# Kernel tuning notes

Hardware: AMD Instinct MI355X
Metric: run time of the kernel (lower is better)

## Reference

```python
import jax, jax.numpy as jnp
import numpy as np
from jax import lax

WS = (4, 8, 8)        # window_size (D,H,W)
DIM = 128
HEADS = 4
HD = DIM // HEADS      # 32
SCALE = HD ** -0.5     # swinv1, lif neuron -> head_dim**-0.5
TAU = 2.0
VTH = 1.0
ALPHA = 2.0            # ATan surrogate width


def _rel_pos_index(ws):
    # static numpy computation of relative_position_index, shape (N, N)
    coords = np.stack(np.meshgrid(np.arange(ws[0]), np.arange(ws[1]), np.arange(ws[2]), indexing='ij'))
    cf = coords.reshape(3, -1)                      # (3, N)
    rel = (cf[:, :, None] - cf[:, None, :]).transpose(1, 2, 0).astype(np.int64)  # (N,N,3)
    rel[:, :, 0] += ws[0] - 1
    rel[:, :, 1] += ws[1] - 1
    rel[:, :, 2] += ws[2] - 1
    rel[:, :, 0] *= (2 * ws[1] - 1) * (2 * ws[2] - 1)
    rel[:, :, 1] *= 2 * ws[2] - 1
    return rel.sum(-1)

RPI = _rel_pos_index(WS)  # (N, N) int


@jax.custom_vjp
def spike(x):
    return (x >= 0.0).astype(x.dtype)

def _spike_fwd(x):
    return spike(x), x

def _spike_bwd(x, g):
    # ATan surrogate gradient (spikingjelly default)
    return (g * (ALPHA / (2.0 * (1.0 + (np.pi / 2.0 * ALPHA * x) ** 2))),)

spike.defvjp(_spike_fwd, _spike_bwd)


def lif(x):
    # multi-step LIF over leading time axis: v' = v + (x - v)/tau, hard reset to 0
    def step(v, xt):
        v = v + (xt - v) / TAU
        s = spike(v - VTH)
        return v * (1.0 - s), s
    return lax.scan(step, jnp.zeros_like(x[0]), x)[1]


def setup_inputs() -> dict:
    key = jax.random.key(0)
    ks = jax.random.split(key, 7)
    x = jax.random.normal(ks[0], (WS[0], 256, WS[1], WS[2], DIM), dtype=jnp.float32)
    Wq = jax.random.normal(ks[1], (DIM, DIM), dtype=jnp.float32) * 0.02
    Wk = jax.random.normal(ks[2], (DIM, DIM), dtype=jnp.float32) * 0.02
    Wv = jax.random.normal(ks[3], (DIM, DIM), dtype=jnp.float32) * 0.02
    rpb_table = jax.random.normal(ks[4], ((2 * WS[0] - 1) * (2 * WS[1] - 1) * (2 * WS[2] - 1), HEADS), dtype=jnp.float32) * 0.02
    Wproj = jax.random.normal(ks[5], (DIM, DIM), dtype=jnp.float32) * 0.02
    bproj = jax.random.normal(ks[6], (DIM,), dtype=jnp.float32) * 0.02
    return {"x": x, "Wq": Wq, "Wk": Wk, "Wv": Wv, "rpb_table": rpb_table, "Wproj": Wproj, "bproj": bproj}


def reference(x, Wq, Wk, Wv, rpb_table, Wproj, bproj):
    T, B_, H, W, C = x.shape
    N = T * H * W
    # QKV: linear (no bias) -> spiking neuron over time axis
    q = lif(jnp.einsum('tbhwc,dc->tbhwd', x, Wq))
    k = lif(jnp.einsum('tbhwc,dc->tbhwd', x, Wk))
    v = lif(jnp.einsum('tbhwc,dc->tbhwd', x, Wv))
    # literal row-major reshape as in torch: (T,B_,H,W,C) -> (B_, heads, N, hd)
    q = q.reshape(B_, HEADS, N, HD)
    k = k.reshape(B_, HEADS, N, HD)
    v = v.reshape(B_, HEADS, N, HD)
    # scaled QK^T (NO softmax in the original forward)
    attn = jnp.einsum('bhnd,bhmd->bhnm', q * SCALE, k)
    rpb = rpb_table[RPI.reshape(-1)].reshape(N, N, HEADS).transpose(2, 0, 1)  # (heads,N,N)
    attn = attn + rpb[None]
    out = jnp.einsum('bhnm,bhmd->bhnd', attn, v)
    out = out.reshape(B_, HEADS, T, H, W, HD).transpose(2, 0, 3, 4, 1, 5).reshape(T, B_, H, W, C)
    out = jnp.einsum('tbhwc,dc->tbhwd', out, Wproj) + bproj
    out = lif(out).reshape(B_, N, C)
    return (out, attn)
```

## Files before the change

kernel.cpp:

```cpp
#include <hip/hip_runtime.h>
#include <hip/hip_bf16.h>


typedef __attribute__((ext_vector_type(8))) short bf16x8;
typedef __attribute__((ext_vector_type(4))) float f32x4;

#define MFMA16(a, b, c) __builtin_amdgcn_mfma_f32_16x16x32_bf16((a), (b), (c), 0, 0, 0)

#define BAR_LDS()                                                \
    do {                                                         \
        asm volatile("s_waitcnt lgkmcnt(0)" ::: "memory");       \
        __builtin_amdgcn_s_barrier();                            \
    } while (0)

__device__ __forceinline__ unsigned short f2bf(float f) {
    union { __hip_bfloat16 h; unsigned short u; } cv;
    cv.h = __float2bfloat16(f);
    return cv.u;
}

__device__ __forceinline__ void cvt8_store(unsigned short* dst, const float* src) {
    float4 f0 = *(const float4*)(src);
    float4 f1 = *(const float4*)(src + 4);
    unsigned short h[8];
    h[0] = f2bf(f0.x); h[1] = f2bf(f0.y); h[2] = f2bf(f0.z); h[3] = f2bf(f0.w);
    h[4] = f2bf(f1.x); h[5] = f2bf(f1.y); h[6] = f2bf(f1.z); h[7] = f2bf(f1.w);
    *(uint4*)dst = *(const uint4*)h;
}

__global__ __launch_bounds__(256) void k_qkv_lif(
    const float* __restrict__ x,
    const float* __restrict__ Wq,
    const float* __restrict__ Wk,
    const float* __restrict__ Wv,
    const float* __restrict__ tbl,
    unsigned int* __restrict__ qbits,
    unsigned int* __restrict__ kbits,
    unsigned int* __restrict__ vbits,
    float* __restrict__ rpbx)
{
    if (blockIdx.y == 3) {
        int base = blockIdx.x * 1024 + threadIdx.x * 4;
        int hh = base >> 16;
        int n = (base >> 8) & 255, m0 = base & 255;
        int zn = n >> 6, yn = (n >> 3) & 7, xn = n & 7;
        float4 o;
#pragma unroll
        for (int i = 0; i < 4; ++i) {
            int m = m0 + i;
            int zm = m >> 6, ym = (m >> 3) & 7, xm = m & 7;
            int ri = (zn - zm + 3) * 225 + (yn - ym + 7) * 15 + (xn - xm + 7);
            ((float*)&o)[i] = tbl[ri * 4 + hh];
        }
        *(float4*)&rpbx[base] = o;
        return;
    }

    __shared__ unsigned short Wl[128 * 136];
    __shared__ unsigned short Xl[64 * 136];

    const int tid = threadIdx.x;
    const int wv = tid >> 6, lane = tid & 63;
    const int l15 = lane & 15, lh = lane >> 4;
    const int wsel = blockIdx.y;
    const float* W = (wsel == 0) ? Wq : (wsel == 1) ? Wk : Wv;
    unsigned int* bits = (wsel == 0) ? qbits : (wsel == 1) ? kbits : vbits;
    const int B = blockIdx.x;

    {
#pragma unroll
        for (int i = 0; i < 8; ++i) {
            int e = i * 2048 + tid * 8;
            int r = e >> 7, cc = e & 127;
            cvt8_store(&Wl[r * 136 + cc], W + r * 128 + cc);
        }
    }

    f32x4 vst[8];
#pragma unroll
    for (int nt = 0; nt < 8; ++nt) vst[nt] = (f32x4){0.f, 0.f, 0.f, 0.f};

    for (int t = 0; t < 4; ++t) {
        BAR_LDS();
        const float* xg = x + t * 2097152 + B * 8192;
#pragma unroll
        for (int i = 0; i < 4; ++i) {
            int e = i * 2048 + tid * 8;
            int r = e >> 7, cc = e & 127;
            cvt8_store(&Xl[r * 136 + cc], xg + r * 128 + cc);
        }
        BAR_LDS();

        f32x4 acc[8];
#pragma unroll
        for (int nt = 0; nt < 8; ++nt) acc[nt] = (f32x4){0.f, 0.f, 0.f, 0.f};
#pragma unroll
        for (int kk = 0; kk < 4; ++kk) {
            bf16x8 a = *(const bf16x8*)&Xl[(wv * 16 + l15) * 136 + kk * 32 + lh * 8];
#pragma unroll
            for (int nt = 0; nt < 8; ++nt) {
                bf16x8 b = *(const bf16x8*)&Wl[(nt * 16 + l15) * 136 + kk * 32 + lh * 8];
                acc[nt] = MFMA16(a, b, acc[nt]);
            }
        }
        unsigned short sp[8][4];
#pragma unroll
        for (int nt = 0; nt < 8; ++nt) {
#pragma unroll
            for (int reg = 0; reg < 4; ++reg) {
                float y = acc[nt][reg];
                float v = vst[nt][reg];
                v = v + (y - v) * 0.5f;
                float s = (v >= 1.0f) ? 1.0f : 0.0f;
                vst[nt][reg] = v * (1.0f - s);
                sp[nt][reg] = (s != 0.0f) ? (unsigned short)1 : (unsigned short)0;
            }
        }
        BAR_LDS();
#pragma unroll
        for (int nt = 0; nt < 8; ++nt)
#pragma unroll
            for (int reg = 0; reg < 4; ++reg)
                Xl[(wv * 16 + lh * 4 + reg) * 136 + nt * 16 + l15] = sp[nt][reg];
        BAR_LDS();
        {
            const unsigned short* rowp = &Xl[(tid >> 2) * 136 + (tid & 3) * 32];
            unsigned int mask = 0;
#pragma unroll
            for (int j8 = 0; j8 < 4; ++j8) {
                uint4 u = *(const uint4*)(rowp + j8 * 8);
                int base = j8 * 8;
                if (u.x & 0xFFFFu) mask |= 1u << (base + 0);
                if (u.x >> 16)     mask |= 1u << (base + 1);
                if (u.y & 0xFFFFu) mask |= 1u << (base + 2);
                if (u.y >> 16)     mask |= 1u << (base + 3);
                if (u.z & 0xFFFFu) mask |= 1u << (base + 4);
                if (u.z >> 16)     mask |= 1u << (base + 5);
                if (u.w & 0xFFFFu) mask |= 1u << (base + 6);
                if (u.w >> 16)     mask |= 1u << (base + 7);
            }
            bits[(t * 256 + B) * 256 + tid] = mask;
        }
    }
}

__global__ __launch_bounds__(256) void k_attn(
    const unsigned int* __restrict__ qbits,
    const unsigned int* __restrict__ kbits,
    const unsigned int* __restrict__ vbits,
    const float* __restrict__ rpbx,
    float* __restrict__ attn_out,
    unsigned short* __restrict__ o_ws)
{
    __shared__ unsigned int  qb[256];
    __shared__ unsigned short vT[32 * 264];
    __shared__ unsigned short attnL[32 * 264];

    const int tid = threadIdx.x;
    const int wv = tid >> 6, lane = tid & 63;
    const int l15 = lane & 15, lh = lane >> 4;
    const int g = blockIdx.x, hh = g & 3;

    qb[tid] = qbits[g * 256 + tid];
    uint4 km = *(const uint4*)&kbits[g * 256 + (tid & 63) * 4];
    {
        unsigned int vb = vbits[g * 256 + tid];
#pragma unroll
        for (int d = 0; d < 32; ++d)
            vT[d * 264 + tid] = ((vb >> d) & 1u) ? (unsigned short)0x3F80
                                                 : (unsigned short)0;
    }
    BAR_LDS();

    const float SC = 0.17677669529663687f;
    float* attn_b = attn_out + (size_t)g * 65536;
    const float* rp = rpbx + hh * 65536;
    unsigned short* ob = o_ws + g * 8192;
    const int rg = wv, m0 = (tid & 63) * 4;
    const int rt = wv >> 1, nh = wv & 1;

    for (int c = 0; c < 8; ++c) {
#pragma unroll
        for (int j = 0; j < 8; ++j) {
            int n = c * 32 + j * 4 + rg;
            unsigned int qn = qb[n];
            float4 rp4 = *(const float4*)&rp[n * 256 + m0];
            f32x4 av;
            av.x = (float)__popc(qn & km.x) * SC + rp4.x;
            av.y = (float)__popc(qn & km.y) * SC + rp4.y;
            av.z = (float)__popc(qn & km.z) * SC + rp4.z;
            av.w = (float)__popc(qn & km.w) * SC + rp4.w;
            __builtin_nontemporal_store(av, (f32x4*)(attn_b + n * 256 + m0));
            unsigned int p0 = (unsigned int)f2bf(av.x) | ((unsigned int)f2bf(av.y) << 16);
            unsigned int p1 = (unsigned int)f2bf(av.z) | ((unsigned int)f2bf(av.w) << 16);
            uint2 pk; pk.x = p0; pk.y = p1;
            *(uint2*)&attnL[(j * 4 + rg) * 264 + m0] = pk;
        }
        BAR_LDS();
        f32x4 oc = (f32x4){0.f, 0.f, 0.f, 0.f};
#pragma unroll
        for (int kk = 0; kk < 8; ++kk) {
            bf16x8 a = *(const bf16x8*)&attnL[(rt * 16 + l15) * 264 + kk * 32 + lh * 8];
            bf16x8 b = *(const bf16x8*)&vT[(nh * 16 + l15) * 264 + kk * 32 + lh * 8];
            oc = MFMA16(a, b, oc);
        }
#pragma unroll
        for (int reg = 0; reg < 4; ++reg) {
            int n = c * 32 + rt * 16 + lh * 4 + reg;
            ob[n * 32 + nh * 16 + l15] = f2bf(oc[reg]);
        }
        BAR_LDS();
    }
}

__global__ __launch_bounds__(256) void k_proj_lif(
    const unsigned short* __restrict__ o_ws,
    const float* __restrict__ Wp,
    const float* __restrict__ bp,
    float* __restrict__ out0)
{
    __shared__ unsigned short Wl[128 * 136];
    __shared__ unsigned short Al[64 * 136];

    const int tid = threadIdx.x;
    const int wv = tid >> 6, lane = tid & 63;
    const int l15 = lane & 15, lh = lane >> 4;
    const int b = blockIdx.x;

    {
#pragma unroll
        for (int i = 0; i < 8; ++i) {
            int e = i * 2048 + tid * 8;
            int r = e >> 7, cc = e & 127;
            cvt8_store(&Wl[r * 136 + cc], Wp + r * 128 + cc);
        }
    }

    float biasf[2];
#pragma unroll
    for (int ntl = 0; ntl < 2; ++ntl)
        biasf[ntl] = bp[(wv * 2 + ntl) * 16 + l15];

    const unsigned short* ob = o_ws + b * 32768;

    for (int c = 0; c < 4; ++c) {
        BAR_LDS();
#pragma unroll
        for (int i = 0; i < 4; ++i) {
            int e = i * 2048 + tid * 8;
            int lr2 = e >> 7, cc = e & 127;
            int t2 = lr2 >> 4, rit = lr2 & 15;
            int hhh = cc >> 5, hd = cc & 31;
            int n = t2 * 64 + c * 16 + rit;
            *(uint4*)&Al[lr2 * 136 + cc] =
                *(const uint4*)(ob + (hhh * 256 + n) * 32 + hd);
        }
        BAR_LDS();

        f32x4 acc[4][2];
#pragma unroll
        for (int t2 = 0; t2 < 4; ++t2)
#pragma unroll
            for (int ntl = 0; ntl < 2; ++ntl)
                acc[t2][ntl] = (f32x4){0.f, 0.f, 0.f, 0.f};
#pragma unroll
        for (int kk = 0; kk < 4; ++kk) {
            bf16x8 a[4];
#pragma unroll
            for (int t2 = 0; t2 < 4; ++t2)
                a[t2] = *(const bf16x8*)&Al[(t2 * 16 + l15) * 136 + kk * 32 + lh * 8];
#pragma unroll
            for (int ntl = 0; ntl < 2; ++ntl) {
                bf16x8 bb = *(const bf16x8*)&Wl[((wv * 2 + ntl) * 16 + l15) * 136 + kk * 32 + lh * 8];
#pragma unroll
                for (int t2 = 0; t2 < 4; ++t2)
                    acc[t2][ntl] = MFMA16(a[t2], bb, acc[t2][ntl]);
            }
        }
#pragma unroll
        for (int ntl = 0; ntl < 2; ++ntl) {
            int d = (wv * 2 + ntl) * 16 + l15;
#pragma unroll
            for (int reg = 0; reg < 4; ++reg) {
                int hw = c * 16 + lh * 4 + reg;
                float v = 0.f;
#pragma unroll
                for (int t2 = 0; t2 < 4; ++t2) {
                    float y = acc[t2][ntl][reg] + biasf[ntl];
                    v = v + (y - v) * 0.5f;
                    float s = (v >= 1.0f) ? 1.0f : 0.0f;
                    v = v * (1.0f - s);
                    __builtin_nontemporal_store(
                        s, out0 + t2 * 2097152 + b * 8192 + hw * 128 + d);
                }
            }
        }
    }
}

extern "C" void kernel_launch(void* const* d_in, const int* in_sizes, int n_in,
                              void* d_out, int out_size, void* d_ws, size_t ws_size,
                              hipStream_t stream)
{
    const float* x   = (const float*)d_in[0];
    const float* Wq  = (const float*)d_in[1];
    const float* Wk  = (const float*)d_in[2];
    const float* Wv  = (const float*)d_in[3];
    const float* tbl = (const float*)d_in[4];
    const float* Wp  = (const float*)d_in[5];
    const float* bp  = (const float*)d_in[6];

    float* out0 = (float*)d_out;
    float* attn = out0 + 8388608;

    unsigned short* o_ws = (unsigned short*)d_ws;
    unsigned int* qbits = (unsigned int*)(o_ws + 8388608);
    unsigned int* kbits = qbits + 262144;
    unsigned int* vbits = kbits + 262144;
    float* rpbx = (float*)(vbits + 262144);

    k_qkv_lif<<<dim3(256, 4), 256, 0, stream>>>(x, Wq, Wk, Wv, tbl,
                                                qbits, kbits, vbits, rpbx);
    k_attn<<<1024, 256, 0, stream>>>(qbits, kbits, vbits, rpbx, attn, o_ws);
    k_proj_lif<<<256, 256, 0, stream>>>(o_ws, Wp, bp, out0);
}
```

Before: 351.6 us.

## Compute relative position bias in-kernel from LDS table instead of expanded buffer

Drops the pre-expanded 4x256x256 relative-position-bias buffer written by the QKV kernel. Each attention block now loads its head's 1575-entry slice of the table into LDS and computes the bias index arithmetically per element. The q bitmasks are read directly from global memory with a wave-uniform row index, so they no longer go through LDS. This removes 1 MB of writes plus repeated global reads of the bias, at the cost of scattered LDS reads and more integer index work per element.

After: 355.3 us. Within noise of the previous version (+1.0%).

```diff
diff --git a/kernel.cpp b/kernel.cpp
--- a/kernel.cpp
+++ b/kernel.cpp
@@ -33,29 +33,10 @@
     const float* __restrict__ Wq,
     const float* __restrict__ Wk,
     const float* __restrict__ Wv,
-    const float* __restrict__ tbl,
     unsigned int* __restrict__ qbits,
     unsigned int* __restrict__ kbits,
-    unsigned int* __restrict__ vbits,
-    float* __restrict__ rpbx)
+    unsigned int* __restrict__ vbits)
 {
-    if (blockIdx.y == 3) {
-        int base = blockIdx.x * 1024 + threadIdx.x * 4;
-        int hh = base >> 16;
-        int n = (base >> 8) & 255, m0 = base & 255;
-        int zn = n >> 6, yn = (n >> 3) & 7, xn = n & 7;
-        float4 o;
-#pragma unroll
-        for (int i = 0; i < 4; ++i) {
-            int m = m0 + i;
-            int zm = m >> 6, ym = (m >> 3) & 7, xm = m & 7;
-            int ri = (zn - zm + 3) * 225 + (yn - ym + 7) * 15 + (xn - xm + 7);
-            ((float*)&o)[i] = tbl[ri * 4 + hh];
-        }
-        *(float4*)&rpbx[base] = o;
-        return;
-    }
-
     __shared__ unsigned short Wl[128 * 136];
     __shared__ unsigned short Xl[64 * 136];
 
@@ -148,20 +129,22 @@
     const unsigned int* __restrict__ qbits,
     const unsigned int* __restrict__ kbits,
     const unsigned int* __restrict__ vbits,
-    const float* __restrict__ rpbx,
+    const float* __restrict__ tbl,
     float* __restrict__ attn_out,
     unsigned short* __restrict__ o_ws)
 {
-    __shared__ unsigned int  qb[256];
     __shared__ unsigned short vT[32 * 264];
     __shared__ unsigned short attnL[32 * 264];
+    __shared__ float tblL[1575];
 
     const int tid = threadIdx.x;
     const int wv = tid >> 6, lane = tid & 63;
     const int l15 = lane & 15, lh = lane >> 4;
     const int g = blockIdx.x, hh = g & 3;
 
-    qb[tid] = qbits[g * 256 + tid];
+    for (int i = tid; i < 1575; i += 256)
+        tblL[i] = tbl[i * 4 + hh];
+
     uint4 km = *(const uint4*)&kbits[g * 256 + (tid & 63) * 4];
     {
         unsigned int vb = vbits[g * 256 + tid];
@@ -170,31 +153,40 @@
             vT[d * 264 + tid] = ((vb >> d) & 1u) ? (unsigned short)0x3F80
                                                  : (unsigned short)0;
     }
+
+    const int m0 = (tid & 63) * 4;
+    int dm[4];
+#pragma unroll
+    for (int i = 0; i < 4; ++i) {
+        int m = m0 + i;
+        dm[i] = (m >> 6) * 225 + ((m >> 3) & 7) * 15 + (m & 7);
+    }
+
     BAR_LDS();
 
     const float SC = 0.17677669529663687f;
     float* attn_b = attn_out + (size_t)g * 65536;
-    const float* rp = rpbx + hh * 65536;
     unsigned short* ob = o_ws + g * 8192;
-    const int rg = wv, m0 = (tid & 63) * 4;
+    const int rowb = __builtin_amdgcn_readfirstlane(wv * 8);
     const int rt = wv >> 1, nh = wv & 1;
 
     for (int c = 0; c < 8; ++c) {
 #pragma unroll
         for (int j = 0; j < 8; ++j) {
-            int n = c * 32 + j * 4 + rg;
-            unsigned int qn = qb[n];
-            float4 rp4 = *(const float4*)&rp[n * 256 + m0];
+            int n = c * 32 + rowb + j;
+            unsigned int qn = qbits[g * 256 + n];
+            int zn = n >> 6, yn = (n >> 3) & 7, xn = n & 7;
+            int basei = zn * 225 + yn * 15 + xn + 787;
             f32x4 av;
-            av.x = (float)__popc(qn & km.x) * SC + rp4.x;
-            av.y = (float)__popc(qn & km.y) * SC + rp4.y;
-            av.z = (float)__popc(qn & km.z) * SC + rp4.z;
-            av.w = (float)__popc(qn & km.w) * SC + rp4.w;
+            av.x = (float)__popc(qn & km.x) * SC + tblL[basei - dm[0]];
+            av.y = (float)__popc(qn & km.y) * SC + tblL[basei - dm[1]];
+            av.z = (float)__popc(qn & km.z) * SC + tblL[basei - dm[2]];
+            av.w = (float)__popc(qn & km.w) * SC + tblL[basei - dm[3]];
             __builtin_nontemporal_store(av, (f32x4*)(attn_b + n * 256 + m0));
             unsigned int p0 = (unsigned int)f2bf(av.x) | ((unsigned int)f2bf(av.y) << 16);
             unsigned int p1 = (unsigned int)f2bf(av.z) | ((unsigned int)f2bf(av.w) << 16);
             uint2 pk; pk.x = p0; pk.y = p1;
-            *(uint2*)&attnL[(j * 4 + rg) * 264 + m0] = pk;
+            *(uint2*)&attnL[(rowb + j) * 264 + m0] = pk;
         }
         BAR_LDS();
         f32x4 oc = (f32x4){0.f, 0.f, 0.f, 0.f};
@@ -317,10 +309,9 @@
     unsigned int* qbits = (unsigned int*)(o_ws + 8388608);
     unsigned int* kbits = qbits + 262144;
     unsigned int* vbits = kbits + 262144;
-    float* rpbx = (float*)(vbits + 262144);
-
-    k_qkv_lif<<<dim3(256, 4), 256, 0, stream>>>(x, Wq, Wk, Wv, tbl,
-                                                qbits, kbits, vbits, rpbx);
-    k_attn<<<1024, 256, 0, stream>>>(qbits, kbits, vbits, rpbx, attn, o_ws);
+
+    k_qkv_lif<<<dim3(256, 3), 256, 0, stream>>>(x, Wq, Wk, Wv,
+                                                qbits, kbits, vbits);
+    k_attn<<<1024, 256, 0, stream>>>(qbits, kbits, vbits, tbl, attn, o_ws);
     k_proj_lif<<<256, 256, 0, stream>>>(o_ws, Wp, bp, out0);
 }
```
